# Performance work log

Measured on AMD Instinct MI355X. Metric: run time of the kernel, lower is better.

Reference implementation:

```python
import jax, jax.numpy as jnp
import numpy as np

EPS = 1e-5

def layernorm(x, gamma, beta):
    mu = jnp.mean(x, axis=-1, keepdims=True)
    var = jnp.var(x, axis=-1, keepdims=True)
    return (x - mu) * jax.lax.rsqrt(var + EPS) * gamma + beta

def setup_inputs() -> dict:
    key = jax.random.key(0)
    ks = jax.random.split(key, 8)
    B, N, D, H, Dh, M = 2, 2048, 768, 12, 64, 3072
    s = 0.02
    return {
        "x": jax.random.normal(ks[0], (B, N, D), jnp.float32),
        "Wqkv": jax.random.normal(ks[1], (D, 3 * H * Dh), jnp.float32) * s,
        "Wout": jax.random.normal(ks[2], (H * Dh, D), jnp.float32) * s,
        "gamma1": jnp.ones((D,), jnp.float32),
        "beta1": jnp.zeros((D,), jnp.float32),
        "gamma2": jnp.ones((D,), jnp.float32),
        "beta2": jnp.zeros((D,), jnp.float32),
        "W1": jax.random.normal(ks[3], (D, M), jnp.float32) * s,
        "b1": jnp.zeros((M,), jnp.float32),
        "W2": jax.random.normal(ks[4], (M, D), jnp.float32) * s,
        "b2": jnp.zeros((D,), jnp.float32),
        "attn_bias": jax.random.normal(ks[5], (1, H, N, N), jnp.float32) * 0.1,
    }

def reference(x, Wqkv, Wout, gamma1, beta1, gamma2, beta2, W1, b1, W2, b2, attn_bias):
    B, N, D = x.shape
    H = attn_bias.shape[1]
    Dh = Wqkv.shape[1] // (3 * H)
    scale = Dh ** -0.5
    # Attention block (pre-norm)
    h = layernorm(x, gamma1, beta1)
    qkv = h @ Wqkv                              # [B, N, 3*H*Dh]
    qkv = qkv.reshape(B, N, 3, H, Dh)
    q, k, v = (jnp.transpose(qkv[:, :, i], (0, 2, 1, 3)) for i in range(3))  # [B, H, N, Dh]
    dots = jnp.einsum('bhqd,bhkd->bhqk', q, k) * scale
    # pos_info == 'mul_att_normed'
    attn = jax.nn.softmax(dots, axis=-1) * jax.nn.softmax(attn_bias, axis=-1)
    attn = attn / jnp.sum(attn, axis=-1, keepdims=True)
    out = jnp.einsum('bhqk,bhkd->bhqd', attn, v)          # [B, H, N, Dh]
    out = jnp.transpose(out, (0, 2, 1, 3)).reshape(B, N, H * Dh)
    x = out @ Wout + x
    # FeedForward block (pre-norm)
    h = layernorm(x, gamma2, beta2)
    h = jax.nn.gelu(h @ W1 + b1, approximate=False)
    x = h @ W2 + b2 + x
    return x
```

## Files before the change

kernel.cpp:

```cpp
#include <hip/hip_runtime.h>

typedef unsigned short u16t;
typedef __bf16 bf16x8 __attribute__((ext_vector_type(8)));
typedef float  f32x4  __attribute__((ext_vector_type(4)));
typedef float  f32x16 __attribute__((ext_vector_type(16)));
typedef unsigned u32x2 __attribute__((ext_vector_type(2)));
typedef unsigned u32x4 __attribute__((ext_vector_type(4)));

#define DEV __device__ __forceinline__

DEV u16t f32_to_bf16(float f) {
    unsigned u = __float_as_uint(f);
    unsigned r = (u + 0x7FFFu + ((u >> 16) & 1u)) >> 16;
    return (u16t)r;
}
DEV float bf16_to_f32(u16t u) { return __uint_as_float((unsigned)u << 16); }

DEV unsigned cvt_pk_bf16(float lo, float hi) {
    unsigned r;
    asm("v_cvt_pk_bf16_f32 %0, %1, %2" : "=v"(r) : "v"(lo), "v"(hi));
    return r;
}

DEV float gelu_exact(float x) {
    return 0.5f * x * (1.0f + erff(x * 0.70710678118654752f));
}

DEV void glds16(const void* g, void* l) {
    __builtin_amdgcn_global_load_lds(
        (const __attribute__((address_space(1))) void*)g,
        (__attribute__((address_space(3))) void*)l, 16, 0, 0);
}

#define SCHED_FENCE() __builtin_amdgcn_sched_barrier(0)

#define WAITN_BARRIER(N)                                          \
    asm volatile("s_waitcnt vmcnt(" #N ")" ::: "memory");         \
    SCHED_FENCE();                                                \
    __builtin_amdgcn_s_barrier();                                 \
    SCHED_FENCE();

#define PLAIN_BARRIER()                                           \
    SCHED_FENCE();                                                \
    __builtin_amdgcn_s_barrier();                                 \
    SCHED_FENCE();

__global__ __launch_bounds__(256)
void ln_kernel(const float* __restrict__ x, const float* __restrict__ g,
               const float* __restrict__ b, u16t* __restrict__ out)
{
    const int row = blockIdx.x;
    const int t = threadIdx.x;
    const float* xr = x + (size_t)row * 768;
    float v0 = xr[t], v1 = xr[t + 256], v2 = xr[t + 512];
    float s = v0 + v1 + v2;
    float s2 = v0 * v0 + v1 * v1 + v2 * v2;
#pragma unroll
    for (int off = 32; off > 0; off >>= 1) {
        s  += __shfl_xor(s, off);
        s2 += __shfl_xor(s2, off);
    }
    __shared__ float sm[8];
    const int w = t >> 6;
    if ((t & 63) == 0) { sm[w] = s; sm[4 + w] = s2; }
    __syncthreads();
    s  = sm[0] + sm[1] + sm[2] + sm[3];
    s2 = sm[4] + sm[5] + sm[6] + sm[7];
    const float mu  = s * (1.0f / 768.0f);
    const float var = fmaxf(s2 * (1.0f / 768.0f) - mu * mu, 0.0f);
    const float rst = rsqrtf(var + 1e-5f);
    u16t* o = out + (size_t)row * 768;
    o[t]       = f32_to_bf16((v0 - mu) * rst * g[t]       + b[t]);
    o[t + 256] = f32_to_bf16((v1 - mu) * rst * g[t + 256] + b[t + 256]);
    o[t + 512] = f32_to_bf16((v2 - mu) * rst * g[t + 512] + b[t + 512]);
}

__global__ __launch_bounds__(256)
void transpose_all(const float* __restrict__ Wqkv, const float* __restrict__ Wout,
                   const float* __restrict__ W1, const float* __restrict__ W2,
                   u16t* __restrict__ WqkvT, u16t* __restrict__ WoutT,
                   u16t* __restrict__ W1T, u16t* __restrict__ W2T)
{
    int b = blockIdx.x;
    const float* in; u16t* out; int R, C, cx, ry;
    if (b < 432)       { in = Wqkv; out = WqkvT; R = 768;  C = 2304; cx = b % 36; ry = b / 36; }
    else if (b < 576)  { b -= 432;  in = Wout; out = WoutT; R = 768;  C = 768;  cx = b % 12; ry = b / 12; }
    else if (b < 1152) { b -= 576;  in = W1;   out = W1T;   R = 768;  C = 3072; cx = b % 48; ry = b / 48; }
    else               { b -= 1152; in = W2;   out = W2T;   R = 3072; C = 768;  cx = b % 12; ry = b / 12; }
    __shared__ float tile[64][65];
    const int c0 = cx * 64, r0 = ry * 64;
    const int t = threadIdx.x;
#pragma unroll
    for (int j = 0; j < 16; ++j) {
        const int idx = j * 256 + t;
        const int rl = idx >> 6, cl = idx & 63;
        tile[rl][cl] = in[(size_t)(r0 + rl) * C + c0 + cl];
    }
    __syncthreads();
#pragma unroll
    for (int j = 0; j < 16; ++j) {
        const int idx = j * 256 + t;
        const int cl = idx >> 6, rl = idx & 63;
        out[(size_t)(c0 + cl) * R + r0 + rl] = f32_to_bf16(tile[rl][cl]);
    }
}

template <int MODE, int TM>
__global__ __launch_bounds__(256)
void gemm_kernel(const u16t* __restrict__ A, const u16t* __restrict__ BT,
                 float* __restrict__ Cf, u16t* __restrict__ Cb,
                 const float* __restrict__ bias, const float* __restrict__ res,
                 u16t* __restrict__ Qo, u16t* __restrict__ Ko,
                 u16t* __restrict__ VTo,
                 int M, int Nn, int K)
{
    constexpr int MI = TM / 32;
    constexpr int ABYTES = TM * 128;
    constexpr int BUFB = ABYTES + 16384;
    __shared__ __align__(16) char gsm[2 * BUFB];
    const int t = threadIdx.x;
    const int w = t >> 6, lane = t & 63;
    const int l16 = lane & 15, lhi = lane >> 4;
    const int wr = w >> 1, wc = w & 1;
    const int m0 = blockIdx.x * TM, n0 = blockIdx.y * 128;

    const f32x4 fz = {0.f, 0.f, 0.f, 0.f};
    f32x4 acc[MI][4];
#pragma unroll
    for (int i = 0; i < MI; ++i)
#pragma unroll
        for (int j = 0; j < 4; ++j) acc[i][j] = fz;

    const int rbase = t >> 3;
    const int ssrc = ((t & 7) ^ (rbase & 7)) * 16;

    auto stage = [&](int bufb, int kt) {
#pragma unroll
        for (int i = 0; i < TM / 32; ++i) {
            const int row = i * 32 + rbase;
            glds16((const char*)A + ((size_t)(m0 + row) * K + kt) * 2 + ssrc,
                   gsm + bufb + i * 4096 + t * 16);
        }
#pragma unroll
        for (int i = 0; i < 4; ++i) {
            const int row = i * 32 + rbase;
            glds16((const char*)BT + ((size_t)(n0 + row) * K + kt) * 2 + ssrc,
                   gsm + bufb + ABYTES + i * 4096 + t * 16);
        }
    };

    auto body = [&](int bufb) {
        const char* Ab = gsm + bufb;
        const char* Bb = gsm + bufb + ABYTES;
#pragma unroll
        for (int ks = 0; ks < 2; ++ks) {
            const int wsl = lhi + 4 * ks;
            bf16x8 af[MI], bfv[4];
#pragma unroll
            for (int i = 0; i < MI; ++i) {
                const int row = 16 * MI * wr + 16 * i + l16;
                af[i] = *reinterpret_cast<const bf16x8*>(
                    Ab + row * 128 + ((wsl ^ (row & 7)) << 4));
            }
#pragma unroll
            for (int j = 0; j < 4; ++j) {
                const int row = 64 * wc + 16 * j + l16;
                bfv[j] = *reinterpret_cast<const bf16x8*>(
                    Bb + row * 128 + ((wsl ^ (row & 7)) << 4));
            }
#pragma unroll
            for (int i = 0; i < MI; ++i)
#pragma unroll
                for (int j = 0; j < 4; ++j)
                    acc[i][j] = __builtin_amdgcn_mfma_f32_16x16x32_bf16(
                        af[i], bfv[j], acc[i][j], 0, 0, 0);
        }
    };

    stage(0, 0);
    int bufb = 0;
    for (int kt = 0; kt + 64 < K; kt += 64) {
        stage(bufb ^ BUFB, kt + 64);
        if constexpr (TM == 128) { WAITN_BARRIER(8) }
        else                     { WAITN_BARRIER(6) }
        body(bufb);
        PLAIN_BARRIER()
        bufb ^= BUFB;
    }
    WAITN_BARRIER(0)
    body(bufb);

    const int rb = m0 + 16 * MI * wr + 4 * lhi;
    const int cb = n0 + 64 * wc + l16;

    if constexpr (MODE == 3) {
        const int qi = n0 / 768;
        const int b = rb >> 11;
        const int nn0 = rb & 2047;
#pragma unroll
        for (int j = 0; j < 4; ++j) {
            const int c = cb - qi * 768 + 16 * j;
            const int h = c >> 6, d = c & 63;
            if (qi < 2) {
                u16t* dst = (qi == 0) ? Qo : Ko;
                const size_t base = ((size_t)(b * 12 + h) * 2048 + nn0) * 64 + d;
#pragma unroll
                for (int i = 0; i < MI; ++i)
#pragma unroll
                    for (int r = 0; r < 4; ++r)
                        dst[base + (size_t)(16 * i + r) * 64] =
                            f32_to_bf16(acc[i][j][r]);
            } else {
                u16t* dst = VTo + ((size_t)(b * 12 + h) * 64 + d) * 2048 + nn0;
#pragma unroll
                for (int i = 0; i < MI; ++i) {
                    u32x2 pr;
                    pr[0] = cvt_pk_bf16(acc[i][j][0], acc[i][j][1]);
                    pr[1] = cvt_pk_bf16(acc[i][j][2], acc[i][j][3]);
                    *reinterpret_cast<u32x2*>(dst + 16 * i) = pr;
                }
            }
        }
        return;
    }

#pragma unroll
    for (int i = 0; i < MI; ++i) {
#pragma unroll
        for (int j = 0; j < 4; ++j) {
#pragma unroll
            for (int r = 0; r < 4; ++r) {
                const int row = rb + 16 * i + r;
                const int col = cb + 16 * j;
                float v = acc[i][j][r];
                if (MODE == 0) {
                    Cf[(size_t)row * Nn + col] = v;
                } else if (MODE == 1) {
                    v += res[(size_t)row * Nn + col];
                    if (bias) v += bias[col];
                    Cf[(size_t)row * Nn + col] = v;
                } else if (MODE == 2) {
                    v = gelu_exact(v + bias[col]);
                    Cb[(size_t)row * Nn + col] = f32_to_bf16(v);
                }
            }
        }
    }
}

__global__ __launch_bounds__(256, 2)
void attn_kernel(const u16t* __restrict__ Q, const u16t* __restrict__ K,
                 const u16t* __restrict__ VT, const float* __restrict__ bias,
                 u16t* __restrict__ Opart, float* __restrict__ Lpart)
{
    const int SEQ = 2048;
    const int h = blockIdx.y;
    const int ks = blockIdx.z;
    const int t = threadIdx.x;
    const int w = t >> 6, lane = t & 63;
    const int l32 = lane & 31, hi = lane >> 5;
    const int q = blockIdx.x * 128 + w * 32 + l32;
    const int bh0 = h, bh1 = 12 + h;

    __shared__ __align__(16) char smem[65536];

    const u16t* qp0 = Q + ((size_t)bh0 * SEQ + q) * 64 + 8 * hi;
    const u16t* qp1 = Q + ((size_t)bh1 * SEQ + q) * 64 + 8 * hi;
    bf16x8 qf0[4], qf1[4];
#pragma unroll
    for (int dseg = 0; dseg < 4; ++dseg) {
        qf0[dseg] = *reinterpret_cast<const bf16x8*>(qp0 + dseg * 16);
        qf1[dseg] = *reinterpret_cast<const bf16x8*>(qp1 + dseg * 16);
    }

    const char* kg0 = (const char*)K + (size_t)bh0 * SEQ * 128;
    const char* kg1 = (const char*)K + (size_t)bh1 * SEQ * 128;
    const char* vg0 = (const char*)VT + (size_t)bh0 * 64 * 4096;
    const char* vg1 = (const char*)VT + (size_t)bh1 * 64 * 4096;
    const char* bg = (const char*)bias +
                     ((size_t)h * SEQ + blockIdx.x * 128) * 8192;

    const int srow8 = lane >> 3;
    const int sslotK = ((lane & 7) ^ srow8) * 16;
    const int vrow  = w * 16 + (lane >> 2);
    const int sslotV = ((lane & 3) ^ ((vrow >> 1) & 3)) * 16;

    auto stage_all = [&](int bb, int k0) {
#pragma unroll
        for (int i = 0; i < 4; ++i) {
            const int row = 32 * w + 8 * i + srow8;
            glds16(bg + (size_t)row * 8192 + (size_t)k0 * 4 + sslotK,
                   smem + bb + 4096 * w + i * 1024);
        }
        glds16(kg0 + (size_t)(k0 + 8 * w + srow8) * 128 + sslotK,
               smem + bb + 16384 + w * 1024);
        glds16(kg1 + (size_t)(k0 + 8 * w + srow8) * 128 + sslotK,
               smem + bb + 20480 + w * 1024);
        glds16(vg0 + (size_t)vrow * 4096 + (size_t)k0 * 2 + sslotV,
               smem + bb + 24576 + w * 1024);
        glds16(vg1 + (size_t)vrow * 4096 + (size_t)k0 * 2 + sslotV,
               smem + bb + 28672 + w * 1024);
    };

    const int rsw = l32 & 7;
    int boff[4], koff[4];
#pragma unroll
    for (int g = 0; g < 4; ++g)
        boff[g] = (32 * w + l32) * 128 + ((((g << 1) + hi) ^ rsw) << 4);
#pragma unroll
    for (int dseg = 0; dseg < 4; ++dseg)
        koff[dseg] = l32 * 128 + ((((dseg << 1) + hi) ^ rsw) << 4);
    const int vr3 = (l32 >> 1) & 3;
    const int voff00 = l32 * 64 + ((hi ^ vr3) << 4);
    const int voff01 = l32 * 64 + (((2 + hi) ^ vr3) << 4);
    const int voff10 = voff00 + 32 * 64;
    const int voff11 = voff01 + 32 * 64;

    f32x16 o00, o01, o10, o11;
#pragma unroll
    for (int i = 0; i < 16; ++i) { o00[i] = 0.f; o01[i] = 0.f;
                                   o10[i] = 0.f; o11[i] = 0.f; }
    float lsum0 = 0.f, lsum1 = 0.f;

    auto batch_body = [&](const bf16x8 (&qf)[4], int kvbase, int vbase,
                          const f32x4 (&bv)[4], f32x16& oa, f32x16& ob,
                          float& lsum) {
        f32x16 st;
#pragma unroll
        for (int i = 0; i < 16; ++i) st[i] = 0.f;
#pragma unroll
        for (int dseg = 0; dseg < 4; ++dseg) {
            bf16x8 kf = *reinterpret_cast<const bf16x8*>(
                smem + kvbase + koff[dseg]);
            st = __builtin_amdgcn_mfma_f32_32x32x16_bf16(kf, qf[dseg], st, 0, 0, 0);
        }
        unsigned pk[8];
#pragma unroll
        for (int i2 = 0; i2 < 8; ++i2) {
            const int ia = 2 * i2, ib = 2 * i2 + 1;
            const float pa = __expf(st[ia] * 0.125f + bv[ia >> 2][ia & 3]);
            const float pb = __expf(st[ib] * 0.125f + bv[ib >> 2][ib & 3]);
            lsum += pa + pb;
            pk[i2] = cvt_pk_bf16(pa, pb);
        }
        unsigned sx[8];
#pragma unroll
        for (int i2 = 0; i2 < 8; ++i2)
            sx[i2] = (unsigned)__shfl_xor((int)pk[i2], 32);
        union { unsigned u[4]; bf16x8 v; } B0, B1;
        B0.u[0] = hi ? sx[2] : pk[0];
        B0.u[1] = hi ? sx[3] : pk[1];
        B0.u[2] = hi ? pk[2] : sx[0];
        B0.u[3] = hi ? pk[3] : sx[1];
        B1.u[0] = hi ? sx[6] : pk[4];
        B1.u[1] = hi ? sx[7] : pk[5];
        B1.u[2] = hi ? pk[6] : sx[4];
        B1.u[3] = hi ? pk[7] : sx[5];
        bf16x8 v00 = *reinterpret_cast<const bf16x8*>(smem + vbase + voff00);
        bf16x8 v01 = *reinterpret_cast<const bf16x8*>(smem + vbase + voff01);
        bf16x8 v10 = *reinterpret_cast<const bf16x8*>(smem + vbase + voff10);
        bf16x8 v11 = *reinterpret_cast<const bf16x8*>(smem + vbase + voff11);
        oa = __builtin_amdgcn_mfma_f32_32x32x16_bf16(v00, B0.v, oa, 0, 0, 0);
        oa = __builtin_amdgcn_mfma_f32_32x32x16_bf16(v01, B1.v, oa, 0, 0, 0);
        ob = __builtin_amdgcn_mfma_f32_32x32x16_bf16(v10, B0.v, ob, 0, 0, 0);
        ob = __builtin_amdgcn_mfma_f32_32x32x16_bf16(v11, B1.v, ob, 0, 0, 0);
    };

    const int kbeg = ks * 512;

    stage_all(0, kbeg);
    WAITN_BARRIER(0)

    int cur = 0;
    for (int i = 0; i < 16; ++i) {
        const int k0 = kbeg + 32 * i;
        if (i < 15) {
            stage_all(cur ^ 32768, k0 + 32);
            WAITN_BARRIER(8)
        } else {
            WAITN_BARRIER(0)
        }
        {
            f32x4 bv[4];
#pragma unroll
            for (int g = 0; g < 4; ++g)
                bv[g] = *reinterpret_cast<const f32x4*>(smem + cur + boff[g]);
            batch_body(qf0, cur + 16384, cur + 24576, bv, o00, o01, lsum0);
            batch_body(qf1, cur + 20480, cur + 28672, bv, o10, o11, lsum1);
        }
        PLAIN_BARRIER()
        cur ^= 32768;
    }

    lsum0 += __shfl_xor(lsum0, 32);
    lsum1 += __shfl_xor(lsum1, 32);

#pragma unroll
    for (int beta = 0; beta < 2; ++beta) {
        const int bh = beta ? bh1 : bh0;
        const f32x16& oa = beta ? o10 : o00;
        const f32x16& ob = beta ? o11 : o01;
        const float ls = beta ? lsum1 : lsum0;
        u16t* op = Opart + ((size_t)(ks * 24 + bh) * SEQ + q) * 64;
#pragma unroll
        for (int dh = 0; dh < 2; ++dh) {
            const f32x16& o = dh ? ob : oa;
#pragma unroll
            for (int g = 0; g < 4; ++g) {
                u32x2 pr;
                pr[0] = cvt_pk_bf16(o[4 * g], o[4 * g + 1]);
                pr[1] = cvt_pk_bf16(o[4 * g + 2], o[4 * g + 3]);
                *reinterpret_cast<u32x2*>(op + dh * 32 + 8 * g + 4 * hi) = pr;
            }
        }
        if (!hi)
            Lpart[(size_t)(ks * 24 + bh) * SEQ + q] = ls;
    }
}

__global__ __launch_bounds__(256)
void attn_combine(const u16t* __restrict__ Opart,
                  const float* __restrict__ Lpart, u16t* __restrict__ out)
{
    const int idx = blockIdx.x * 256 + threadIdx.x;
    const int dg = idx & 7;
    const int q = (idx >> 3) & 2047;
    const int bh = idx >> 14;
    const int b = bh / 12, h = bh % 12;
    const size_t base = ((size_t)bh * 2048 + q) * 64 + dg * 8;
    const size_t stride = (size_t)24 * 2048 * 64;
    float acc[8] = {0.f, 0.f, 0.f, 0.f, 0.f, 0.f, 0.f, 0.f};
    float l = 0.f;
#pragma unroll
    for (int j = 0; j < 4; ++j) {
        const u32x4 a = *reinterpret_cast<const u32x4*>(Opart + base + j * stride);
#pragma unroll
        for (int m = 0; m < 4; ++m) {
            acc[2 * m]     += bf16_to_f32((u16t)(a[m] & 0xFFFF));
            acc[2 * m + 1] += bf16_to_f32((u16t)(a[m] >> 16));
        }
        l += Lpart[(size_t)j * 24 * 2048 + bh * 2048 + q];
    }
    const float inv = 1.0f / l;
    u32x4 r;
#pragma unroll
    for (int m = 0; m < 4; ++m)
        r[m] = cvt_pk_bf16(acc[2 * m] * inv, acc[2 * m + 1] * inv);
    *reinterpret_cast<u32x4*>(
        out + ((size_t)(b * 2048 + q)) * 768 + h * 64 + dg * 8) = r;
}

extern "C" void kernel_launch(void* const* d_in, const int* in_sizes, int n_in,
                              void* d_out, int out_size, void* d_ws, size_t ws_size,
                              hipStream_t stream)
{
    const float* x    = (const float*)d_in[0];
    const float* Wqkv = (const float*)d_in[1];
    const float* Wout = (const float*)d_in[2];
    const float* g1   = (const float*)d_in[3];
    const float* be1  = (const float*)d_in[4];
    const float* g2   = (const float*)d_in[5];
    const float* be2  = (const float*)d_in[6];
    const float* W1   = (const float*)d_in[7];
    const float* b1   = (const float*)d_in[8];
    const float* W2   = (const float*)d_in[9];
    const float* b2   = (const float*)d_in[10];
    const float* ab   = (const float*)d_in[11];
    float* outp = (float*)d_out;

    char* ws = (char*)d_ws;
    size_t off = 0;
    auto alloc = [&](size_t bytes) -> char* {
        char* p = ws + off;
        off += (bytes + 255) & ~(size_t)255;
        return p;
    };

    u16t* WqkvT = (u16t*)alloc((size_t)2304 * 768 * 2);
    u16t* WoutT = (u16t*)alloc((size_t)768 * 768 * 2);
    u16t* W1T   = (u16t*)alloc((size_t)3072 * 768 * 2);
    u16t* W2T   = (u16t*)alloc((size_t)768 * 3072 * 2);
    u16t* h1    = (u16t*)alloc((size_t)4096 * 768 * 2);
    u16t* Qb    = (u16t*)alloc((size_t)24 * 2048 * 64 * 2);
    u16t* Kb    = (u16t*)alloc((size_t)24 * 2048 * 64 * 2);
    u16t* VTb   = (u16t*)alloc((size_t)24 * 64 * 2048 * 2);
    u16t* attnb = (u16t*)alloc((size_t)4096 * 768 * 2);
    float* x1   = (float*)alloc((size_t)4096 * 768 * 4);
    u16t* h2    = (u16t*)alloc((size_t)4096 * 768 * 2);
    u16t* Opart = (u16t*)alloc((size_t)4 * 24 * 2048 * 64 * 2);
    float* Lpart = (float*)alloc((size_t)4 * 24 * 2048 * 4);
    u16t* act   = (u16t*)alloc((size_t)4096 * 3072 * 2);

    transpose_all<<<1728, 256, 0, stream>>>(Wqkv, Wout, W1, W2,
                                            WqkvT, WoutT, W1T, W2T);

    ln_kernel<<<4096, 256, 0, stream>>>(x, g1, be1, h1);
    gemm_kernel<3, 128><<<dim3(32, 18), 256, 0, stream>>>(
        h1, WqkvT, nullptr, nullptr, nullptr, nullptr, Qb, Kb, VTb,
        4096, 2304, 768);
    attn_kernel<<<dim3(16, 12, 4), 256, 0, stream>>>(Qb, Kb, VTb, ab, Opart, Lpart);
    attn_combine<<<(24 * 2048 * 8) / 256, 256, 0, stream>>>(Opart, Lpart, attnb);
    gemm_kernel<1, 64><<<dim3(64, 6), 256, 0, stream>>>(
        attnb, WoutT, x1, nullptr, nullptr, x, nullptr, nullptr, nullptr,
        4096, 768, 768);

    ln_kernel<<<4096, 256, 0, stream>>>(x1, g2, be2, h2);
    gemm_kernel<2, 128><<<dim3(32, 24), 256, 0, stream>>>(
        h2, W1T, nullptr, act, b1, nullptr, nullptr, nullptr, nullptr,
        4096, 3072, 768);
    gemm_kernel<1, 64><<<dim3(64, 6), 256, 0, stream>>>(
        act, W2T, outp, nullptr, b2, x1, nullptr, nullptr, nullptr,
        4096, 768, 3072);
}
```

Baseline: 226.9 us.

## Vectorize layernorm with 192 threads and single-buffer GEMM LDS staging

The layernorm kernel now uses 192 threads, each loading a float4 and storing four packed bf16 values. The GEMM kernel drops LDS double buffering and the prefetch pipeline in favour of a simple load, sync, compute, sync loop. This halves GEMM LDS use, which may allow more resident blocks, but global loads no longer overlap MFMA compute.

```diff
diff --git a/kernel.cpp b/kernel.cpp
--- a/kernel.cpp
+++ b/kernel.cpp
@@ -45,34 +45,37 @@
     __builtin_amdgcn_s_barrier();                                 \
     SCHED_FENCE();
 
-__global__ __launch_bounds__(256)
+__global__ __launch_bounds__(192)
 void ln_kernel(const float* __restrict__ x, const float* __restrict__ g,
                const float* __restrict__ b, u16t* __restrict__ out)
 {
     const int row = blockIdx.x;
     const int t = threadIdx.x;
-    const float* xr = x + (size_t)row * 768;
-    float v0 = xr[t], v1 = xr[t + 256], v2 = xr[t + 512];
-    float s = v0 + v1 + v2;
-    float s2 = v0 * v0 + v1 * v1 + v2 * v2;
+    const f32x4 v = *reinterpret_cast<const f32x4*>(x + (size_t)row * 768 + t * 4);
+    float s  = v[0] + v[1] + v[2] + v[3];
+    float s2 = v[0] * v[0] + v[1] * v[1] + v[2] * v[2] + v[3] * v[3];
 #pragma unroll
     for (int off = 32; off > 0; off >>= 1) {
         s  += __shfl_xor(s, off);
         s2 += __shfl_xor(s2, off);
     }
-    __shared__ float sm[8];
+    __shared__ float sm[6];
     const int w = t >> 6;
-    if ((t & 63) == 0) { sm[w] = s; sm[4 + w] = s2; }
+    if ((t & 63) == 0) { sm[w] = s; sm[3 + w] = s2; }
     __syncthreads();
-    s  = sm[0] + sm[1] + sm[2] + sm[3];
-    s2 = sm[4] + sm[5] + sm[6] + sm[7];
+    s  = sm[0] + sm[1] + sm[2];
+    s2 = sm[3] + sm[4] + sm[5];
     const float mu  = s * (1.0f / 768.0f);
     const float var = fmaxf(s2 * (1.0f / 768.0f) - mu * mu, 0.0f);
     const float rst = rsqrtf(var + 1e-5f);
-    u16t* o = out + (size_t)row * 768;
-    o[t]       = f32_to_bf16((v0 - mu) * rst * g[t]       + b[t]);
-    o[t + 256] = f32_to_bf16((v1 - mu) * rst * g[t + 256] + b[t + 256]);
-    o[t + 512] = f32_to_bf16((v2 - mu) * rst * g[t + 512] + b[t + 512]);
+    const f32x4 gv = *reinterpret_cast<const f32x4*>(g + t * 4);
+    const f32x4 bv = *reinterpret_cast<const f32x4*>(b + t * 4);
+    u32x2 r;
+    r[0] = cvt_pk_bf16((v[0] - mu) * rst * gv[0] + bv[0],
+                       (v[1] - mu) * rst * gv[1] + bv[1]);
+    r[1] = cvt_pk_bf16((v[2] - mu) * rst * gv[2] + bv[2],
+                       (v[3] - mu) * rst * gv[3] + bv[3]);
+    *reinterpret_cast<u32x2*>(out + (size_t)row * 768 + t * 4) = r;
 }
 
 __global__ __launch_bounds__(256)
@@ -116,8 +119,7 @@
 {
     constexpr int MI = TM / 32;
     constexpr int ABYTES = TM * 128;
-    constexpr int BUFB = ABYTES + 16384;
-    __shared__ __align__(16) char gsm[2 * BUFB];
+    __shared__ __align__(16) char gsm[ABYTES + 16384];
     const int t = threadIdx.x;
     const int w = t >> 6, lane = t & 63;
     const int l16 = lane & 15, lhi = lane >> 4;
@@ -134,24 +136,24 @@
     const int rbase = t >> 3;
     const int ssrc = ((t & 7) ^ (rbase & 7)) * 16;
 
-    auto stage = [&](int bufb, int kt) {
+    auto stage = [&](int kt) {
 #pragma unroll
         for (int i = 0; i < TM / 32; ++i) {
             const int row = i * 32 + rbase;
             glds16((const char*)A + ((size_t)(m0 + row) * K + kt) * 2 + ssrc,
-                   gsm + bufb + i * 4096 + t * 16);
+                   gsm + i * 4096 + t * 16);
         }
 #pragma unroll
         for (int i = 0; i < 4; ++i) {
             const int row = i * 32 + rbase;
             glds16((const char*)BT + ((size_t)(n0 + row) * K + kt) * 2 + ssrc,
-                   gsm + bufb + ABYTES + i * 4096 + t * 16);
+                   gsm + ABYTES + i * 4096 + t * 16);
         }
     };
 
-    auto body = [&](int bufb) {
-        const char* Ab = gsm + bufb;
-        const char* Bb = gsm + bufb + ABYTES;
+    auto body = [&]() {
+        const char* Ab = gsm;
+        const char* Bb = gsm + ABYTES;
 #pragma unroll
         for (int ks = 0; ks < 2; ++ks) {
             const int wsl = lhi + 4 * ks;
@@ -177,18 +179,12 @@
         }
     };
 
-    stage(0, 0);
-    int bufb = 0;
-    for (int kt = 0; kt + 64 < K; kt += 64) {
-        stage(bufb ^ BUFB, kt + 64);
-        if constexpr (TM == 128) { WAITN_BARRIER(8) }
-        else                     { WAITN_BARRIER(6) }
-        body(bufb);
-        PLAIN_BARRIER()
-        bufb ^= BUFB;
-    }
-    WAITN_BARRIER(0)
-    body(bufb);
+    for (int kt = 0; kt < K; kt += 64) {
+        stage(kt);
+        __syncthreads();
+        body();
+        __syncthreads();
+    }
 
     const int rb = m0 + 16 * MI * wr + 4 * lhi;
     const int cb = n0 + 64 * wc + l16;
@@ -494,7 +490,7 @@
     transpose_all<<<1728, 256, 0, stream>>>(Wqkv, Wout, W1, W2,
                                             WqkvT, WoutT, W1T, W2T);
 
-    ln_kernel<<<4096, 256, 0, stream>>>(x, g1, be1, h1);
+    ln_kernel<<<4096, 192, 0, stream>>>(x, g1, be1, h1);
     gemm_kernel<3, 128><<<dim3(32, 18), 256, 0, stream>>>(
         h1, WqkvT, nullptr, nullptr, nullptr, nullptr, Qb, Kb, VTb,
         4096, 2304, 768);
@@ -504,7 +500,7 @@
         attnb, WoutT, x1, nullptr, nullptr, x, nullptr, nullptr, nullptr,
         4096, 768, 768);
 
-    ln_kernel<<<4096, 256, 0, stream>>>(x1, g2, be2, h2);
+    ln_kernel<<<4096, 192, 0, stream>>>(x1, g2, be2, h2);
     gemm_kernel<2, 128><<<dim3(32, 24), 256, 0, stream>>>(
         h2, W1T, nullptr, act, b1, nullptr, nullptr, nullptr, nullptr,
         4096, 3072, 768);
```

Result: faster. 221.9 us (-2.2%).
